# Kernel tuning notes

Hardware: AMD Instinct MI355X
Metric: run time of the kernel (lower is better)

The kernel has to match this reference:

```python
import jax, jax.numpy as jnp
import numpy as np

PC = 512      # proposal_channels == conv_channels
INCH = 512    # in_channels of branch
B = 8
T = 64        # pyramid level length (feat_t) at order=0
TF = 256      # frame_level_feature length (clip_length)
KERNELS = [8, 16, 8, 4, 2, 2, 2]  # ConPoolingKernal
CLC = 498     # feature_lastclass channels (CLC + 2 == 500)
GROUPS = 32


def _gn(x, gamma, beta):
    # GroupNorm(32, C) over [B, C, L]
    Bb, C, L = x.shape
    xg = x.reshape(Bb, GROUPS, C // GROUPS, L)
    m = xg.mean(axis=(2, 3), keepdims=True)
    v = xg.var(axis=(2, 3), keepdims=True)
    xn = ((xg - m) * jax.lax.rsqrt(v + 1e-5)).reshape(Bb, C, L)
    return xn * gamma[None, :, None] + beta[None, :, None]


def _c1(x, w, b):
    # Unit1D kernel_shape=1: pointwise conv
    return jnp.einsum('bct,oc->bot', x, w) + b[None, :, None]


def _bmp(feat, segs):
    # BoundaryMaxPooling: first C/2 channels max-pooled over segs[...,0:2],
    # second C/2 over segs[...,2:4] (inclusive integer ranges, clamped).
    Bb, C, L = feat.shape
    C2 = C // 2
    pos = jnp.arange(L)
    def pool(f, s, e):
        s = jnp.clip(s, 0, L - 1)
        e = jnp.maximum(jnp.clip(e, 0, L - 1), s)
        mask = (pos[None, None, :] >= s[..., None]) & (pos[None, None, :] <= e[..., None])  # [B,T,L]
        return jnp.max(jnp.where(mask[:, None], f[:, :, None, :], -jnp.inf), axis=-1)  # [B,C2,T]
    return jnp.concatenate([pool(feat[:, :C2], segs[..., 0], segs[..., 1]),
                            pool(feat[:, C2:], segs[..., 2], segs[..., 3])], axis=1)


def _anchor_gather(feat, anc, K):
    # Vectorized per-anchor clamp/slice + nearest F.interpolate(size=K):
    # src index for output k of a slice [l, r] is l + floor(k * (r - l + 1) / K).
    Bb, C, L = feat.shape
    left = jnp.clip(anc[..., 0], 0, L)
    right = jnp.clip(anc[..., 1], 0, L)
    valid = right > left                      # empty slices -> zeros (torch branch)
    seglen = right + 1 - left
    k = jnp.arange(K)
    idx = jnp.clip(left[..., None] + (k[None, None, :] * seglen[..., None]) // K, 0, L - 1)  # [B,T,K]
    g = jax.vmap(lambda f, ix: f[:, ix])(feat, idx)   # [B,C,T,K]
    return g * valid[:, None, :, None].astype(feat.dtype)


def setup_inputs() -> dict:
    key = jax.random.key(0)
    ks = jax.random.split(key, 16)
    f32 = jnp.float32
    s = 0.02
    def w(k, shape):
        return jax.random.normal(k, shape, f32) * s
    inp = {}
    inp['feature'] = jax.random.normal(ks[0], (B, INCH, T), f32)
    inp['frame_level_feature'] = jax.random.normal(ks[1], (B, PC, TF), f32)
    inp['segments'] = jax.random.randint(ks[2], (B, T, 4), 0, T).astype(jnp.int32)
    inp['frame_segments'] = jax.random.randint(ks[3], (B, T, 4), 0, TF).astype(jnp.int32)
    inp['feature_lastclass'] = jax.random.normal(ks[4], (B, CLC, T), f32)
    inp['anchor'] = jnp.sort(jax.random.randint(ks[5], (B, T, 2), 0, T), axis=-1).astype(jnp.int32)
    inp['frame_anchor'] = jnp.sort(jax.random.randint(ks[6], (B, T, 2), 0, TF), axis=-1).astype(jnp.int32)
    inp['order'] = 0
    inp['LocResult_feature'] = jax.random.normal(ks[7], (B, 2, T), f32)
    inp['w_cur'] = w(ks[8], (PC, INCH)); inp['b_cur'] = jnp.zeros((PC,), f32)
    inp['g_cur'] = jnp.ones((PC,), f32); inp['be_cur'] = jnp.zeros((PC,), f32)
    inp['w_lr'] = w(ks[9], (2 * PC, INCH)); inp['b_lr'] = jnp.zeros((2 * PC,), f32)
    inp['g_lr'] = jnp.ones((2 * PC,), f32); inp['be_lr'] = jnp.zeros((2 * PC,), f32)
    inp['w_roi'] = w(ks[10], (PC, PC)); inp['b_roi'] = jnp.zeros((PC,), f32)
    inp['g_roi'] = jnp.ones((PC,), f32); inp['be_roi'] = jnp.zeros((PC,), f32)
    K1 = KERNELS[1]; K0 = KERNELS[0]
    inp['w_cp'] = w(ks[11], (PC, 2 * PC, K1)); inp['b_cp'] = jnp.zeros((PC,), f32)
    inp['w_cp0'] = w(ks[12], (PC, PC, K0)); inp['b_cp0'] = jnp.zeros((PC,), f32)
    CIN = 6 * PC + 500
    inp['w_prop'] = w(ks[13], (INCH, CIN)); inp['b_prop'] = jnp.zeros((INCH,), f32)
    inp['g_prop'] = jnp.ones((INCH,), f32); inp['be_prop'] = jnp.zeros((INCH,), f32)
    return inp


def reference(feature, frame_level_feature, segments, frame_segments, feature_lastclass,
              anchor, frame_anchor, order, LocResult_feature,
              w_cur, b_cur, g_cur, be_cur, w_lr, b_lr, g_lr, be_lr,
              w_roi, b_roi, g_roi, be_roi, w_cp, b_cp, w_cp0, b_cp0,
              w_prop, b_prop, g_prop, be_prop):
    relu = jax.nn.relu
    fm_short = relu(_gn(_c1(feature, w_cur, b_cur), g_cur, be_cur))           # [B,PC,T]
    feat_lr = relu(_gn(_c1(feature, w_lr, b_lr), g_lr, be_lr))                # [B,2PC,T]
    prop_feature = _bmp(feat_lr, segments)                                    # [B,2PC,T]
    prop_roi = relu(_gn(_c1(_bmp(frame_level_feature, frame_segments), w_roi, b_roi), g_roi, be_roi))
    K1 = KERNELS[order + 1]
    K0 = KERNELS[0]
    g1 = _anchor_gather(feat_lr, anchor, K1)                                  # [B,2PC,T,K1]
    con_feature = jnp.einsum('bctk,ock->bot', g1, w_cp) + b_cp[None, :, None]  # valid conv K1->1
    g0 = _anchor_gather(frame_level_feature, frame_anchor, K0)                # [B,PC,T,K0]
    frame_con = jnp.einsum('bctk,ock->bot', g0, w_cp0) + b_cp0[None, :, None]
    prop_con = relu(_gn(_c1(frame_con, w_roi, b_roi), g_roi, be_roi))
    cat = jnp.concatenate([prop_roi, prop_feature, fm_short, feature_lastclass,
                           con_feature, prop_con, LocResult_feature], axis=1)  # [B,6PC+500,T]
    out = relu(_gn(_c1(cat, w_prop, b_prop), g_prop, be_prop))                # [B,INCH,T]
    return (out, feat_lr)
```

## Files before the change

### kernel.cpp

```cpp
#include <hip/hip_runtime.h>
#include <math.h>

#define BB 8
#define CATP 3584
#define CAT_REAL 3572

typedef __attribute__((ext_vector_type(8))) short short8;
typedef __attribute__((ext_vector_type(4))) float f32x4;

__device__ inline ushort f2bf(float f) {
  union { float f; unsigned u; } x;
  x.f = f;
  return (ushort)((x.u + 0x7FFFu + ((x.u >> 16) & 1u)) >> 16);
}
__device__ inline float bf2f(unsigned us) {
  union { unsigned u; float f; } x;
  x.u = us << 16;
  return x.f;
}

template <int Cin, int Kf>
__device__ void cpT_tile(const float* __restrict__ W, ushort* __restrict__ D,
                         int nt, int cc) {
  const int tid = threadIdx.x;
  const int j = tid >> 6, l4 = (tid >> 4) & 3, l15 = tid & 15;
  const int o = nt * 64 + j * 16 + l15;
  const int cb = cc * 32 + l4 * 8;
  ushort rg[8][Kf];
#pragma unroll
  for (int q = 0; q < 8; q++) {
    const float* row = W + ((size_t)o * Cin + cb + q) * Kf;
#pragma unroll
    for (int kq = 0; kq < Kf / 4; kq++) {
      const float4 f = *(const float4*)(row + kq * 4);
      rg[q][kq * 4 + 0] = f2bf(f.x);
      rg[q][kq * 4 + 1] = f2bf(f.y);
      rg[q][kq * 4 + 2] = f2bf(f.z);
      rg[q][kq * 4 + 3] = f2bf(f.w);
    }
  }
#pragma unroll
  for (int k = 0; k < Kf; k++) {
    uint4 pk;
    pk.x = (unsigned)rg[0][k] | ((unsigned)rg[1][k] << 16);
    pk.y = (unsigned)rg[2][k] | ((unsigned)rg[3][k] << 16);
    pk.z = (unsigned)rg[4][k] | ((unsigned)rg[5][k] << 16);
    pk.w = (unsigned)rg[6][k] | ((unsigned)rg[7][k] << 16);
    *(uint4*)(D + ((size_t)(nt * Kf + k) * (Cin >> 5) + cc) * 2048 + tid * 8) = pk;
  }
}

__global__ __launch_bounds__(256) void prep_kernel(
    const float* __restrict__ w_cur, const float* __restrict__ w_lr,
    const float* __restrict__ w_roi, const float* __restrict__ w_prop,
    ushort* __restrict__ Wcomb, ushort* __restrict__ Wroi,
    ushort* __restrict__ Wprop, const float* __restrict__ w_cp,
    ushort* __restrict__ WcpT, const float* __restrict__ w_cp0,
    ushort* __restrict__ Wcp0T, const float* __restrict__ feature,
    const float* __restrict__ frame_feat, const float* __restrict__ lastcls,
    const float* __restrict__ locres, ushort* __restrict__ Ft,
    ushort* __restrict__ FfT, ushort* __restrict__ cat) {
  __shared__ float tile[64 * 65];
  const int bid = blockIdx.x;
  if (bid < 1408) {
    const int i = bid * 256 + threadIdx.x;
    const float* src;
    ushort* dst;
    int o, k8, Kc;
    bool pad = false;
    if (i < 98304) {
      o = i >> 6; k8 = i & 63; Kc = 16;
      src = (o < 512) ? (w_cur + (size_t)o * 512)
                      : (w_lr + (size_t)(o - 512) * 512);
      dst = Wcomb;
    } else if (i < 131072) {
      const int r = i - 98304;
      o = r >> 6; k8 = r & 63; Kc = 16;
      src = w_roi + (size_t)o * 512;
      dst = Wroi;
    } else {
      const int r = i - 131072;
      if (r >= 229376) return;
      o = r / 448; k8 = r % 448; Kc = 112;
      src = w_prop + (size_t)o * CAT_REAL;
      dst = Wprop;
      pad = true;
    }
    const int k = k8 * 8;
    float v[8];
    if (pad) {
#pragma unroll
      for (int q = 0; q < 8; q++) v[q] = (k + q < CAT_REAL) ? src[k + q] : 0.f;
    } else {
      const float4 f0 = *(const float4*)(src + k);
      const float4 f1 = *(const float4*)(src + k + 4);
      v[0] = f0.x; v[1] = f0.y; v[2] = f0.z; v[3] = f0.w;
      v[4] = f1.x; v[5] = f1.y; v[6] = f1.z; v[7] = f1.w;
    }
    uint4 pk;
    pk.x = (unsigned)f2bf(v[0]) | ((unsigned)f2bf(v[1]) << 16);
    pk.y = (unsigned)f2bf(v[2]) | ((unsigned)f2bf(v[3]) << 16);
    pk.z = (unsigned)f2bf(v[4]) | ((unsigned)f2bf(v[5]) << 16);
    pk.w = (unsigned)f2bf(v[6]) | ((unsigned)f2bf(v[7]) << 16);
    const int ot = o >> 6, ii = (o >> 4) & 3, l15 = o & 15;
    const int kc = k8 >> 2, l4 = k8 & 3;
    const size_t flat =
        ((((size_t)ot * Kc + kc) * 4 + ii) * 64 + l4 * 16 + l15) * 8;
    *(uint4*)(dst + flat) = pk;
    return;
  }
  if (bid < 1792) {
    const int local = bid - 1408;
    if (local < 256)
      cpT_tile<1024, 16>(w_cp, WcpT, local >> 5, local & 31);
    else {
      const int r = local - 256;
      cpT_tile<512, 8>(w_cp0, Wcp0T, r >> 4, r & 15);
    }
    return;
  }
  const int local = bid - 1792;
  const float* src;
  ushort* dst;
  int Cr, Cw, L, rs, co, cblk, lblk, b;
  if (local < 64) {
    src = feature; dst = Ft; Cr = 512; Cw = 512; L = 64; rs = 512; co = 0;
    cblk = local & 7; lblk = 0; b = local >> 3;
  } else if (local < 320) {
    const int r = local - 64;
    src = frame_feat; dst = FfT; Cr = 512; Cw = 512; L = 256; rs = 512; co = 0;
    cblk = r & 7; lblk = (r >> 3) & 3; b = r >> 5;
  } else if (local < 384) {
    const int r = local - 320;
    src = lastcls; dst = cat; Cr = 498; Cw = 498; L = 64; rs = CATP; co = 2048;
    cblk = r & 7; lblk = 0; b = r >> 3;
  } else {
    const int r = local - 384;
    src = locres; dst = cat; Cr = 2; Cw = 14; L = 64; rs = CATP; co = 3570;
    cblk = 0; lblk = 0; b = r;
  }
  const int c0 = cblk * 64, l0 = lblk * 64;
  for (int e = threadIdx.x; e < 4096; e += 256) {
    const int cc = e >> 6, ll = e & 63;
    const int c = c0 + cc;
    tile[cc * 65 + ll] = (c < Cr) ? src[((size_t)b * Cr + c) * L + l0 + ll] : 0.f;
  }
  __syncthreads();
  for (int e = threadIdx.x; e < 4096; e += 256) {
    const int ll = e >> 6, cc = e & 63;
    const int c = c0 + cc;
    if (c < Cw)
      dst[((size_t)b * L + l0 + ll) * rs + co + c] = f2bf(tile[cc * 65 + ll]);
  }
}

__device__ void gemm_gn_body(const ushort* __restrict__ Xt,
                             const ushort* __restrict__ Wb,
                             const float* __restrict__ bias,
                             const float* __restrict__ gamma,
                             const float* __restrict__ beta, int Kp,
                             int cpgShift, float* __restrict__ outF, int outFM,
                             ushort* __restrict__ catOut, int catStride,
                             int chOff, int ot, int b, float* smem) {
  float* red = smem;
  float* rs = smem + 4224;
  float* rss = smem + 4228;
  float* gmean = smem + 4232;
  float* grstd = smem + 4236;
  const int w = threadIdx.x >> 6;
  const int lane = threadIdx.x & 63;
  const int l15 = lane & 15, l4 = lane >> 4;
  const int o0 = ot * 64;

  f32x4 acc[4] = {};
  const ushort* wbase = Wb + (size_t)ot * (Kp >> 5) * 2048 + lane * 8;
  const ushort* bp[4];
#pragma unroll
  for (int j = 0; j < 4; j++)
    bp[j] = Xt + (size_t)(b * 64 + j * 16 + l15) * Kp + l4 * 8;
  const int nkc = Kp >> 5;
  for (int kc = 0; kc < nkc; kc++) {
    const short8 a = *(const short8*)(wbase + ((size_t)kc * 4 + w) * 512);
    short8 x[4];
#pragma unroll
    for (int j = 0; j < 4; j++) x[j] = *(const short8*)(bp[j] + kc * 32);
#pragma unroll
    for (int j = 0; j < 4; j++)
      acc[j] = __builtin_amdgcn_mfma_f32_16x16x32_bf16(a, x[j], acc[j], 0, 0, 0);
  }
#pragma unroll
  for (int j = 0; j < 4; j++)
#pragma unroll
    for (int r = 0; r < 4; r++) {
      const int m = w * 16 + l4 * 4 + r;
      red[m * 65 + j * 16 + l15] = acc[j][r] + bias[o0 + m];
    }
  __syncthreads();

  const int cpg = 1 << cpgShift;
  const int ngroups = 64 >> cpgShift;
  for (int gi = 0; gi < ngroups; gi++) {
    float s = 0.f, ss = 0.f;
    const int nel = cpg << 6;
    for (int e = threadIdx.x; e < nel; e += 256) {
      const float v = red[((gi << cpgShift) + (e >> 6)) * 65 + (e & 63)];
      s += v;
      ss += v * v;
    }
#pragma unroll
    for (int off = 32; off > 0; off >>= 1) {
      s += __shfl_down(s, off);
      ss += __shfl_down(ss, off);
    }
    if (lane == 0) { rs[w] = s; rss[w] = ss; }
    __syncthreads();
    if (threadIdx.x == 0) {
      const float ts = rs[0] + rs[1] + rs[2] + rs[3];
      const float tss = rss[0] + rss[1] + rss[2] + rss[3];
      const float mean = ts / (float)nel;
      const float var = tss / (float)nel - mean * mean;
      gmean[gi] = mean;
      grstd[gi] = rsqrtf(var + 1e-5f);
    }
    __syncthreads();
  }

  if (outF) {
    for (int e = threadIdx.x; e < 4096; e += 256) {
      const int m = e >> 6, n = e & 63;
      const int gi = m >> cpgShift;
      const int c = o0 + m;
      float v = (red[m * 65 + n] - gmean[gi]) * grstd[gi] * gamma[c] + beta[c];
      v = fmaxf(v, 0.f);
      outF[((size_t)b * outFM + c) * 64 + n] = v;
    }
  }
  if (catOut) {
    for (int e = threadIdx.x; e < 4096; e += 256) {
      const int n = e >> 6, m = e & 63;
      const int gi = m >> cpgShift;
      const int c = o0 + m;
      float v = (red[m * 65 + n] - gmean[gi]) * grstd[gi] * gamma[c] + beta[c];
      v = fmaxf(v, 0.f);
      catOut[((size_t)(b * 64) + n) * catStride + chOff + c] = f2bf(v);
    }
  }
}

__device__ void gemm_part_body(const ushort* __restrict__ Xt,
                               const ushort* __restrict__ Wb,
                               float* __restrict__ P, int ot, int b, int slice,
                               int kbeg, int kend) {
  const int w = threadIdx.x >> 6;
  const int lane = threadIdx.x & 63;
  const int l15 = lane & 15, l4 = lane >> 4;
  f32x4 acc[4] = {};
  const ushort* wbase = Wb + (size_t)ot * (CATP >> 5) * 2048 + lane * 8;
  const ushort* bp[4];
#pragma unroll
  for (int j = 0; j < 4; j++)
    bp[j] = Xt + (size_t)(b * 64 + j * 16 + l15) * CATP + l4 * 8;
  for (int k = kbeg; k < kend; k += 32) {
    const int kc = k >> 5;
    const short8 a = *(const short8*)(wbase + ((size_t)kc * 4 + w) * 512);
    short8 x[4];
#pragma unroll
    for (int j = 0; j < 4; j++) x[j] = *(const short8*)(bp[j] + k);
#pragma unroll
    for (int j = 0; j < 4; j++)
      acc[j] = __builtin_amdgcn_mfma_f32_16x16x32_bf16(a, x[j], acc[j], 0, 0, 0);
  }
  float* Pp = P + (((size_t)slice * BB + b) * 512 + ot * 64) * 64;
#pragma unroll
  for (int j = 0; j < 4; j++)
#pragma unroll
    for (int r = 0; r < 4; r++)
      Pp[(w * 16 + l4 * 4 + r) * 64 + j * 16 + l15] = acc[j][r];
}

__global__ __launch_bounds__(256) void reduce_gn_kernel(
    const float* __restrict__ P, const float* __restrict__ bias,
    const float* __restrict__ gamma, const float* __restrict__ beta,
    float* __restrict__ outF) {
  const int ot = blockIdx.x;
  const int b = blockIdx.y;
  const int o0 = ot * 64;
  const int w = threadIdx.x >> 6;
  const int lane = threadIdx.x & 63;
  __shared__ float red[64 * 65];
  for (int e = threadIdx.x; e < 4096; e += 256) {
    const int m = e >> 6, n = e & 63;
    float s = bias[o0 + m];
#pragma unroll
    for (int z = 0; z < 4; z++)
      s += P[(((size_t)z * BB + b) * 512 + o0 + m) * 64 + n];
    red[m * 65 + n] = s;
  }
  __syncthreads();
  __shared__ float rs[4], rss[4], gmean[4], grstd[4];
  for (int gi = 0; gi < 4; gi++) {
    float s = 0.f, ss = 0.f;
    for (int e = threadIdx.x; e < 1024; e += 256) {
      const float v = red[((gi << 4) + (e >> 6)) * 65 + (e & 63)];
      s += v;
      ss += v * v;
    }
#pragma unroll
    for (int off = 32; off > 0; off >>= 1) {
      s += __shfl_down(s, off);
      ss += __shfl_down(ss, off);
    }
    if (lane == 0) { rs[w] = s; rss[w] = ss; }
    __syncthreads();
    if (threadIdx.x == 0) {
      const float ts = rs[0] + rs[1] + rs[2] + rs[3];
      const float tss = rss[0] + rss[1] + rss[2] + rss[3];
      const float mean = ts / 1024.f;
      const float var = tss / 1024.f - mean * mean;
      gmean[gi] = mean;
      grstd[gi] = rsqrtf(var + 1e-5f);
    }
    __syncthreads();
  }
  for (int e = threadIdx.x; e < 4096; e += 256) {
    const int m = e >> 6, n = e & 63;
    const int gi = m >> 4;
    const int c = o0 + m;
    float v = (red[m * 65 + n] - gmean[gi]) * grstd[gi] * gamma[c] + beta[c];
    outF[((size_t)b * 512 + c) * 64 + n] = fmaxf(v, 0.f);
  }
}

template <int C, int L>
__device__ void bmp_body(const ushort* __restrict__ Xt,
                         const int* __restrict__ segs, ushort* __restrict__ Y,
                         int rowStride, int chOff, int t, int b,
                         float2 (*pmax)[512]) {
  constexpr int C2 = C / 2;
  constexpr int P2 = C2 / 2;
  constexpr int CH = P2 / 64;
  const int w = threadIdx.x >> 6;
  const int lane = threadIdx.x & 63;
  const int* sg = segs + ((size_t)b * 64 + t) * 4;
  const ushort* Xb = Xt + (size_t)b * L * C;
#pragma unroll
  for (int h = 0; h < 2; h++) {
    const int s = min(max(sg[2 * h], 0), L - 1);
    const int e = max(min(max(sg[2 * h + 1], 0), L - 1), s);
#pragma unroll
    for (int q = 0; q < CH; q++) {
      const int p = q * 64 + lane;
      const ushort* base = Xb + h * C2 + 2 * p;
      float a0 = -INFINITY, a1 = -INFINITY;
      float c0 = -INFINITY, c1 = -INFINITY;
      int l = s + w;
      for (; l + 4 <= e; l += 8) {
        const unsigned u0 = *(const unsigned*)(base + (size_t)l * C);
        const unsigned u1 = *(const unsigned*)(base + (size_t)(l + 4) * C);
        a0 = fmaxf(a0, bf2f(u0 & 0xffffu));
        a1 = fmaxf(a1, bf2f(u0 >> 16));
        c0 = fmaxf(c0, bf2f(u1 & 0xffffu));
        c1 = fmaxf(c1, bf2f(u1 >> 16));
      }
      if (l <= e) {
        const unsigned u0 = *(const unsigned*)(base + (size_t)l * C);
        a0 = fmaxf(a0, bf2f(u0 & 0xffffu));
        a1 = fmaxf(a1, bf2f(u0 >> 16));
      }
      pmax[w][h * P2 + p] = make_float2(fmaxf(a0, c0), fmaxf(a1, c1));
    }
  }
  __syncthreads();
  for (int idx = threadIdx.x; idx < 2 * P2; idx += 256) {
    float2 m = pmax[0][idx];
#pragma unroll
    for (int ww = 1; ww < 4; ww++) {
      const float2 v = pmax[ww][idx];
      m.x = fmaxf(m.x, v.x);
      m.y = fmaxf(m.y, v.y);
    }
    const unsigned o = (unsigned)f2bf(m.x) | ((unsigned)f2bf(m.y) << 16);
    *(unsigned*)(Y + ((size_t)(b * 64) + t) * rowStride + chOff + 2 * idx) = o;
  }
}

template <int Kf, int L, int Cin, int NT>
__device__ void anchor_body2(const ushort* __restrict__ src,
                             const int* __restrict__ anc,
                             const ushort* __restrict__ Wt,
                             float* __restrict__ P, int nt, int b, int slice) {
  const int w = threadIdx.x >> 6;
  const int lane = threadIdx.x & 63;
  const int l15 = lane & 15, l4 = lane >> 4;
  const int t = w * 16 + l15;
  const int a0 = anc[((size_t)b * 64 + t) * 2 + 0];
  const int a1 = anc[((size_t)b * 64 + t) * 2 + 1];
  const int left = min(max(a0, 0), L);
  const int right = min(max(a1, 0), L);
  const int seglen = right + 1 - left;

  f32x4 acc[4] = {};
#pragma unroll
  for (int kt = 0; kt < NT; kt++) {
    const int k = slice * NT + kt;
    const int ix = min(max(left + (k * seglen) / Kf, 0), L - 1);
    const ushort* rp = src + ((size_t)b * L + ix) * Cin + l4 * 8;
    const ushort* wb = Wt + ((size_t)nt * Kf + k) * (Cin >> 5) * 2048 + lane * 8;
#pragma unroll 4
    for (int c0 = 0; c0 < Cin; c0 += 32) {
      const int cc = c0 >> 5;
      const short8 a = *(const short8*)(rp + c0);
      short8 bbf[4];
#pragma unroll
      for (int j = 0; j < 4; j++)
        bbf[j] = *(const short8*)(wb + ((size_t)cc * 4 + j) * 512);
#pragma unroll
      for (int j = 0; j < 4; j++)
        acc[j] =
            __builtin_amdgcn_mfma_f32_16x16x32_bf16(a, bbf[j], acc[j], 0, 0, 0);
    }
  }
  float* Pp = P + (((size_t)slice * BB + b) * 64) * 512 + nt * 64;
#pragma unroll
  for (int j = 0; j < 4; j++)
#pragma unroll
    for (int r = 0; r < 4; r++)
      Pp[(size_t)(w * 16 + l4 * 4 + r) * 512 + j * 16 + l15] = acc[j][r];
}

__device__ void anchor_reduce_body(const float* __restrict__ P, int ks,
                                   const float* __restrict__ bias,
                                   const int* __restrict__ anc, int L,
                                   ushort* __restrict__ Y, int rowStride,
                                   int chOff, int ot, int b, float* smem) {
  float* tile = smem;
  float* sval = smem + 4160;
  const int o0 = ot * 64;
  if (threadIdx.x < 64) {
    const int t = threadIdx.x;
    const int a0 = anc[((size_t)b * 64 + t) * 2 + 0];
    const int a1 = anc[((size_t)b * 64 + t) * 2 + 1];
    const int left = min(max(a0, 0), L);
    const int right = min(max(a1, 0), L);
    sval[t] = (right > left) ? 1.f : 0.f;
  }
  __syncthreads();
  for (int e = threadIdx.x; e < 4096; e += 256) {
    const int m = e >> 6, nl = e & 63;
    float s = 0.f;
    for (int z = 0; z < ks; z++)
      s += P[(((size_t)z * BB + b) * 64 + m) * 512 + o0 + nl];
    tile[nl * 65 + m] = s * sval[m] + bias[o0 + nl];
  }
  __syncthreads();
  for (int e = threadIdx.x; e < 4096; e += 256) {
    const int m = e >> 6, nl = e & 63;
    Y[((size_t)(b * 64) + m) * rowStride + chOff + o0 + nl] =
        f2bf(tile[nl * 65 + m]);
  }
}

__global__ __launch_bounds__(256) void fused_B_kernel(
    const ushort* __restrict__ Ft, const ushort* __restrict__ Wcomb,
    const float* __restrict__ b_cur, const float* __restrict__ g_cur,
    const float* __restrict__ be_cur, ushort* __restrict__ cat,
    const float* __restrict__ b_lr, const float* __restrict__ g_lr,
    const float* __restrict__ be_lr, float* __restrict__ feat_lr,
    ushort* __restrict__ FlrT, const ushort* __restrict__ FfT,
    const int* __restrict__ frame_segs, ushort* __restrict__ XbmpT,
    const int* __restrict__ frame_anchor, const ushort* __restrict__ Wcp0T,
    float* __restrict__ P0) {
  __shared__ __align__(16) float smem[4240];
  const int bid = blockIdx.x;
  if (bid < 128) {
    const int nt = bid & 7, b = (bid >> 3) & 7, slice = bid >> 6;
    anchor_body2<8, 256, 512, 4>(FfT, frame_anchor, Wcp0T, P0, nt, b, slice);
  } else if (bid < 320) {
    const int r = bid - 128;
    const int b = r / 24, ot24 = r % 24;
    if (ot24 < 8)
      gemm_gn_body(Ft, Wcomb, b_cur, g_cur, be_cur, 512, 4, nullptr, 0, cat,
                   CATP, 1536, ot24, b, smem);
    else
      gemm_gn_body(Ft, Wcomb + 512 * 512, b_lr, g_lr, be_lr, 512, 5, feat_lr,
                   1024, FlrT, 1024, 0, ot24 - 8, b, smem);
  } else {
    const int r = bid - 320;
    bmp_body<512, 256>(FfT, frame_segs, XbmpT, 512, 0, r & 63, r >> 6,
                       (float2(*)[512])smem);
  }
}

__global__ __launch_bounds__(256) void fused_C_kernel(
    const ushort* __restrict__ FlrT, const int* __restrict__ segments,
    ushort* __restrict__ cat, const int* __restrict__ anchor,
    const ushort* __restrict__ WcpT, float* __restrict__ P1,
    const float* __restrict__ P0, const float* __restrict__ b_cp0,
    const int* __restrict__ frame_anchor, ushort* __restrict__ FconT,
    const ushort* __restrict__ XbmpT, const ushort* __restrict__ Wroi,
    const float* __restrict__ b_roi, const float* __restrict__ g_roi,
    const float* __restrict__ be_roi) {
  __shared__ __align__(16) float smem[4240];
  const int bid = blockIdx.x;
  if (bid < 256) {
    const int nt = bid & 7, b = (bid >> 3) & 7, slice = bid >> 6;
    anchor_body2<16, 64, 1024, 4>(FlrT, anchor, WcpT, P1, nt, b, slice);
  } else if (bid < 320) {
    const int r = bid - 256;
    gemm_gn_body(XbmpT, Wroi, b_roi, g_roi, be_roi, 512, 4, nullptr, 0, cat,
                 CATP, 0, r & 7, r >> 3, smem);
  } else if (bid < 384) {
    const int r = bid - 320;
    anchor_reduce_body(P0, 2, b_cp0, frame_anchor, 256, FconT, 512, 0, r & 7,
                       r >> 3, smem);
  } else {
    const int r = bid - 384;
    bmp_body<1024, 64>(FlrT, segments, cat, CATP, 512, r & 63, r >> 6,
                       (float2(*)[512])smem);
  }
}

__global__ __launch_bounds__(256) void fused_D_kernel(
    const ushort* __restrict__ cat, const ushort* __restrict__ Wprop,
    float* __restrict__ P9, const float* __restrict__ P1,
    const float* __restrict__ b_cp, const int* __restrict__ anchor,
    ushort* __restrict__ catw, const ushort* __restrict__ FconT,
    const ushort* __restrict__ Wroi, const float* __restrict__ b_roi,
    const float* __restrict__ g_roi, const float* __restrict__ be_roi) {
  __shared__ __align__(16) float smem[4240];
  const int bid = blockIdx.x;
  if (bid < 192) {
    const int s = bid >> 6, q = bid & 63;
    const int kb = (s == 0) ? 0 : (s == 1) ? 864 : 1728;
    const int ke = (s == 0) ? 864 : (s == 1) ? 1728 : 2528;
    gemm_part_body(cat, Wprop, P9, q & 7, q >> 3, s, kb, ke);
  } else if (bid < 256) {
    const int r = bid - 192;
    anchor_reduce_body(P1, 4, b_cp, anchor, 64, catw, CATP, 2546, r & 7,
                       r >> 3, smem);
  } else {
    const int r = bid - 256;
    gemm_gn_body(FconT, Wroi, b_roi, g_roi, be_roi, 512, 4, nullptr, 0, catw,
                 CATP, 3058, r & 7, r >> 3, smem);
  }
}

__global__ __launch_bounds__(256) void part_E_kernel(
    const ushort* __restrict__ cat, const ushort* __restrict__ Wprop,
    float* __restrict__ P9) {
  gemm_part_body(cat, Wprop, P9, blockIdx.x & 7, blockIdx.x >> 3, 3, 2528,
                 3584);
}

extern "C" void kernel_launch(void* const* d_in, const int* in_sizes, int n_in,
                              void* d_out, int out_size, void* d_ws,
                              size_t ws_size, hipStream_t stream) {
  const float* feature      = (const float*)d_in[0];
  const float* frame_feat   = (const float*)d_in[1];
  const int*   segments     = (const int*)d_in[2];
  const int*   frame_segs   = (const int*)d_in[3];
  const float* feat_lastcls = (const float*)d_in[4];
  const int*   anchor       = (const int*)d_in[5];
  const int*   frame_anchor = (const int*)d_in[6];
  const float* locres       = (const float*)d_in[8];
  const float* w_cur  = (const float*)d_in[9];
  const float* b_cur  = (const float*)d_in[10];
  const float* g_cur  = (const float*)d_in[11];
  const float* be_cur = (const float*)d_in[12];
  const float* w_lr   = (const float*)d_in[13];
  const float* b_lr   = (const float*)d_in[14];
  const float* g_lr   = (const float*)d_in[15];
  const float* be_lr  = (const float*)d_in[16];
  const float* w_roi  = (const float*)d_in[17];
  const float* b_roi  = (const float*)d_in[18];
  const float* g_roi  = (const float*)d_in[19];
  const float* be_roi = (const float*)d_in[20];
  const float* w_cp   = (const float*)d_in[21];
  const float* b_cp   = (const float*)d_in[22];
  const float* w_cp0  = (const float*)d_in[23];
  const float* b_cp0  = (const float*)d_in[24];
  const float* w_prop = (const float*)d_in[25];
  const float* b_prop = (const float*)d_in[26];
  const float* g_prop = (const float*)d_in[27];
  const float* be_prop= (const float*)d_in[28];

  float* out_main = (float*)d_out;
  float* feat_lr  = (float*)d_out + BB * 512 * 64;

  ushort* cat_t  = (ushort*)d_ws;
  ushort* Ft     = cat_t + 1835008;
  ushort* XbmpT  = Ft + 262144;
  ushort* FconT  = XbmpT + 262144;
  ushort* Wcomb  = FconT + 262144;
  ushort* Wroi   = Wcomb + 786432;
  ushort* Wprop  = Wroi + 262144;
  ushort* WcpT   = Wprop + 1835008;
  ushort* Wcp0T  = WcpT + 8388608;
  ushort* FlrT   = Wcp0T + 2097152;
  ushort* FfT    = FlrT + 524288;
  float*  P1     = (float*)(FfT + 1048576);
  float*  P0     = P1 + 2097152;
  float*  P9     = P0 + 1048576;

  prep_kernel<<<2184, 256, 0, stream>>>(
      w_cur, w_lr, w_roi, w_prop, Wcomb, Wroi, Wprop, w_cp, WcpT, w_cp0,
      Wcp0T, feature, frame_feat, feat_lastcls, locres, Ft, FfT, cat_t);

  fused_B_kernel<<<832, 256, 0, stream>>>(
      Ft, Wcomb, b_cur, g_cur, be_cur, cat_t, b_lr, g_lr, be_lr, feat_lr,
      FlrT, FfT, frame_segs, XbmpT, frame_anchor, Wcp0T, P0);

  fused_C_kernel<<<896, 256, 0, stream>>>(
      FlrT, segments, cat_t, anchor, WcpT, P1, P0, b_cp0, frame_anchor, FconT,
      XbmpT, Wroi, b_roi, g_roi, be_roi);

  fused_D_kernel<<<320, 256, 0, stream>>>(
      cat_t, Wprop, P9, P1, b_cp, anchor, cat_t, FconT, Wroi, b_roi, g_roi,
      be_roi);

  part_E_kernel<<<64, 256, 0, stream>>>(cat_t, Wprop, P9);

  reduce_gn_kernel<<<dim3(8, BB), 256, 0, stream>>>(
      P9, b_prop, g_prop, be_prop, out_main);
}
```

Measured before the change: 326.9 us.

## Split anchor conv work finer and fold last prop GEMM slice into GN reduce

The anchor-gather convolutions are split into more blocks: one tap per block for frame anchors, and two taps with half the channels per block for level anchors. This raises parallelism but writes more partial buffers, which the reduce stages must then sum (8 and 16 partials). The final prop GEMM K-slice is moved from a separate kernel into the GroupNorm reduce kernel, removing one launch. In exchange, that reduce kernel now runs serial MFMA work on only 64 blocks, and the workspace partial buffers double in size.

```diff
diff --git a/kernel.cpp b/kernel.cpp
--- a/kernel.cpp
+++ b/kernel.cpp
@@ -279,6 +279,7 @@
 }
 
 __global__ __launch_bounds__(256) void reduce_gn_kernel(
+    const ushort* __restrict__ cat, const ushort* __restrict__ Wprop,
     const float* __restrict__ P, const float* __restrict__ bias,
     const float* __restrict__ gamma, const float* __restrict__ beta,
     float* __restrict__ outF) {
@@ -287,14 +288,39 @@
   const int o0 = ot * 64;
   const int w = threadIdx.x >> 6;
   const int lane = threadIdx.x & 63;
+  const int l15 = lane & 15, l4 = lane >> 4;
+
+  f32x4 acc[4] = {};
+  const ushort* wbase = Wprop + (size_t)ot * (CATP >> 5) * 2048 + lane * 8;
+  const ushort* bp[4];
+#pragma unroll
+  for (int j = 0; j < 4; j++)
+    bp[j] = cat + (size_t)(b * 64 + j * 16 + l15) * CATP + l4 * 8;
+  for (int k = 2528; k < 3584; k += 32) {
+    const int kc = k >> 5;
+    const short8 a = *(const short8*)(wbase + ((size_t)kc * 4 + w) * 512);
+    short8 x[4];
+#pragma unroll
+    for (int j = 0; j < 4; j++) x[j] = *(const short8*)(bp[j] + k);
+#pragma unroll
+    for (int j = 0; j < 4; j++)
+      acc[j] = __builtin_amdgcn_mfma_f32_16x16x32_bf16(a, x[j], acc[j], 0, 0, 0);
+  }
+
   __shared__ float red[64 * 65];
+#pragma unroll
+  for (int j = 0; j < 4; j++)
+#pragma unroll
+    for (int r = 0; r < 4; r++)
+      red[(w * 16 + l4 * 4 + r) * 65 + j * 16 + l15] = acc[j][r];
+  __syncthreads();
   for (int e = threadIdx.x; e < 4096; e += 256) {
     const int m = e >> 6, n = e & 63;
     float s = bias[o0 + m];
 #pragma unroll
     for (int z = 0; z < 4; z++)
       s += P[(((size_t)z * BB + b) * 512 + o0 + m) * 64 + n];
-    red[m * 65 + n] = s;
+    red[m * 65 + n] += s;
   }
   __syncthreads();
   __shared__ float rs[4], rss[4], gmean[4], grstd[4];
@@ -384,11 +410,12 @@
   }
 }
 
-template <int Kf, int L, int Cin, int NT>
+template <int Kf, int L, int Cin, int NT, int CSPAN>
 __device__ void anchor_body2(const ushort* __restrict__ src,
                              const int* __restrict__ anc,
                              const ushort* __restrict__ Wt,
-                             float* __restrict__ P, int nt, int b, int slice) {
+                             float* __restrict__ P, int nt, int b, int tapbase,
+                             int cbase, int slice) {
   const int w = threadIdx.x >> 6;
   const int lane = threadIdx.x & 63;
   const int l15 = lane & 15, l4 = lane >> 4;
@@ -402,13 +429,13 @@
   f32x4 acc[4] = {};
 #pragma unroll
   for (int kt = 0; kt < NT; kt++) {
-    const int k = slice * NT + kt;
+    const int k = tapbase + kt;
     const int ix = min(max(left + (k * seglen) / Kf, 0), L - 1);
-    const ushort* rp = src + ((size_t)b * L + ix) * Cin + l4 * 8;
+    const ushort* rp = src + ((size_t)b * L + ix) * Cin + cbase + l4 * 8;
     const ushort* wb = Wt + ((size_t)nt * Kf + k) * (Cin >> 5) * 2048 + lane * 8;
 #pragma unroll 4
-    for (int c0 = 0; c0 < Cin; c0 += 32) {
-      const int cc = c0 >> 5;
+    for (int c0 = 0; c0 < CSPAN; c0 += 32) {
+      const int cc = (cbase + c0) >> 5;
       const short8 a = *(const short8*)(rp + c0);
       short8 bbf[4];
 #pragma unroll
@@ -472,11 +499,12 @@
     float* __restrict__ P0) {
   __shared__ __align__(16) float smem[4240];
   const int bid = blockIdx.x;
-  if (bid < 128) {
-    const int nt = bid & 7, b = (bid >> 3) & 7, slice = bid >> 6;
-    anchor_body2<8, 256, 512, 4>(FfT, frame_anchor, Wcp0T, P0, nt, b, slice);
-  } else if (bid < 320) {
-    const int r = bid - 128;
+  if (bid < 512) {
+    const int nt = bid & 7, b = (bid >> 3) & 7, s = bid >> 6;
+    anchor_body2<8, 256, 512, 1, 512>(FfT, frame_anchor, Wcp0T, P0, nt, b, s,
+                                      0, s);
+  } else if (bid < 704) {
+    const int r = bid - 512;
     const int b = r / 24, ot24 = r % 24;
     if (ot24 < 8)
       gemm_gn_body(Ft, Wcomb, b_cur, g_cur, be_cur, 512, 4, nullptr, 0, cat,
@@ -485,7 +513,7 @@
       gemm_gn_body(Ft, Wcomb + 512 * 512, b_lr, g_lr, be_lr, 512, 5, feat_lr,
                    1024, FlrT, 1024, 0, ot24 - 8, b, smem);
   } else {
-    const int r = bid - 320;
+    const int r = bid - 704;
     bmp_body<512, 256>(FfT, frame_segs, XbmpT, 512, 0, r & 63, r >> 6,
                        (float2(*)[512])smem);
   }
@@ -502,19 +530,21 @@
     const float* __restrict__ be_roi) {
   __shared__ __align__(16) float smem[4240];
   const int bid = blockIdx.x;
-  if (bid < 256) {
-    const int nt = bid & 7, b = (bid >> 3) & 7, slice = bid >> 6;
-    anchor_body2<16, 64, 1024, 4>(FlrT, anchor, WcpT, P1, nt, b, slice);
-  } else if (bid < 320) {
-    const int r = bid - 256;
+  if (bid < 1024) {
+    const int nt = bid & 7, b = (bid >> 3) & 7, s = bid >> 6;
+    const int kz = s >> 1, ch = s & 1;
+    anchor_body2<16, 64, 1024, 2, 512>(FlrT, anchor, WcpT, P1, nt, b, kz * 2,
+                                       ch * 512, s);
+  } else if (bid < 1088) {
+    const int r = bid - 1024;
     gemm_gn_body(XbmpT, Wroi, b_roi, g_roi, be_roi, 512, 4, nullptr, 0, cat,
                  CATP, 0, r & 7, r >> 3, smem);
-  } else if (bid < 384) {
-    const int r = bid - 320;
-    anchor_reduce_body(P0, 2, b_cp0, frame_anchor, 256, FconT, 512, 0, r & 7,
+  } else if (bid < 1152) {
+    const int r = bid - 1088;
+    anchor_reduce_body(P0, 8, b_cp0, frame_anchor, 256, FconT, 512, 0, r & 7,
                        r >> 3, smem);
   } else {
-    const int r = bid - 384;
+    const int r = bid - 1152;
     bmp_body<1024, 64>(FlrT, segments, cat, CATP, 512, r & 63, r >> 6,
                        (float2(*)[512])smem);
   }
@@ -529,27 +559,20 @@
     const float* __restrict__ g_roi, const float* __restrict__ be_roi) {
   __shared__ __align__(16) float smem[4240];
   const int bid = blockIdx.x;
-  if (bid < 192) {
+  if (bid < 256) {
     const int s = bid >> 6, q = bid & 63;
-    const int kb = (s == 0) ? 0 : (s == 1) ? 864 : 1728;
-    const int ke = (s == 0) ? 864 : (s == 1) ? 1728 : 2528;
+    const int kb = s * 640;
+    const int ke = (s == 3) ? 2528 : kb + 640;
     gemm_part_body(cat, Wprop, P9, q & 7, q >> 3, s, kb, ke);
-  } else if (bid < 256) {
-    const int r = bid - 192;
-    anchor_reduce_body(P1, 4, b_cp, anchor, 64, catw, CATP, 2546, r & 7,
+  } else if (bid < 320) {
+    const int r = bid - 256;
+    anchor_reduce_body(P1, 16, b_cp, anchor, 64, catw, CATP, 2546, r & 7,
                        r >> 3, smem);
   } else {
-    const int r = bid - 256;
+    const int r = bid - 320;
     gemm_gn_body(FconT, Wroi, b_roi, g_roi, be_roi, 512, 4, nullptr, 0, catw,
                  CATP, 3058, r & 7, r >> 3, smem);
   }
-}
-
-__global__ __launch_bounds__(256) void part_E_kernel(
-    const ushort* __restrict__ cat, const ushort* __restrict__ Wprop,
-    float* __restrict__ P9) {
-  gemm_part_body(cat, Wprop, P9, blockIdx.x & 7, blockIdx.x >> 3, 3, 2528,
-                 3584);
 }
 
 extern "C" void kernel_launch(void* const* d_in, const int* in_sizes, int n_in,
@@ -599,27 +622,25 @@
   ushort* FlrT   = Wcp0T + 2097152;
   ushort* FfT    = FlrT + 524288;
   float*  P1     = (float*)(FfT + 1048576);
-  float*  P0     = P1 + 2097152;
-  float*  P9     = P0 + 1048576;
+  float*  P0     = P1 + 4194304;
+  float*  P9     = P0 + 2097152;
 
   prep_kernel<<<2184, 256, 0, stream>>>(
       w_cur, w_lr, w_roi, w_prop, Wcomb, Wroi, Wprop, w_cp, WcpT, w_cp0,
       Wcp0T, feature, frame_feat, feat_lastcls, locres, Ft, FfT, cat_t);
 
-  fused_B_kernel<<<832, 256, 0, stream>>>(
+  fused_B_kernel<<<1216, 256, 0, stream>>>(
       Ft, Wcomb, b_cur, g_cur, be_cur, cat_t, b_lr, g_lr, be_lr, feat_lr,
       FlrT, FfT, frame_segs, XbmpT, frame_anchor, Wcp0T, P0);
 
-  fused_C_kernel<<<896, 256, 0, stream>>>(
+  fused_C_kernel<<<1664, 256, 0, stream>>>(
       FlrT, segments, cat_t, anchor, WcpT, P1, P0, b_cp0, frame_anchor, FconT,
       XbmpT, Wroi, b_roi, g_roi, be_roi);
 
-  fused_D_kernel<<<320, 256, 0, stream>>>(
+  fused_D_kernel<<<384, 256, 0, stream>>>(
       cat_t, Wprop, P9, P1, b_cp, anchor, cat_t, FconT, Wroi, b_roi, g_roi,
       be_roi);
 
-  part_E_kernel<<<64, 256, 0, stream>>>(cat_t, Wprop, P9);
-
   reduce_gn_kernel<<<dim3(8, BB), 256, 0, stream>>>(
-      P9, b_prop, g_prop, be_prop, out_main);
-}
+      cat_t, Wprop, P9, b_prop, g_prop, be_prop, out_main);
+}
```

Measured after the change: 298.2 us. 1.1x faster.
